# Kernel tuning notes

Measured on AMD Instinct MI355X. Metric: run time of the kernel, lower is better.

## Reference

```python
import jax, jax.numpy as jnp
import numpy as np

B, S, D = 2, 2048, 4096
NH, NKV = 32, 8
HD = D // NH          # 128
NREP = NH // NKV      # 4
SCALE = HD ** -0.5


def setup_inputs() -> dict:
    key = jax.random.key(0)
    kx, kq, kk, kv, ko = jax.random.split(key, 5)
    s = 0.02
    return {
        "x": jax.random.normal(kx, (B, S, D), dtype=jnp.float32),
        "wq": jax.random.normal(kq, (D, NH * HD), dtype=jnp.float32) * s,
        "wk": jax.random.normal(kk, (D, NKV * HD), dtype=jnp.float32) * s,
        "wv": jax.random.normal(kv, (D, NKV * HD), dtype=jnp.float32) * s,
        "wo": jax.random.normal(ko, (NH * HD, D), dtype=jnp.float32) * s,
    }


def reference(x, wq, wk, wv, wo):
    b, s, _ = x.shape
    q = (x @ wq).reshape(b, s, NH, HD)    # b s h d
    k = (x @ wk).reshape(b, s, NKV, HD)   # b s kv d
    v = (x @ wv).reshape(b, s, NKV, HD)
    # GQA: repeat kv heads to match query heads
    k = jnp.repeat(k, NREP, axis=2)       # b s h d
    v = jnp.repeat(v, NREP, axis=2)
    scores = jnp.einsum("bihd,bjhd->bhij", q, k) * SCALE  # b h i j
    causal = jnp.tril(jnp.ones((s, s), dtype=bool))
    scores = jnp.where(causal, scores, jnp.finfo(scores.dtype).min)
    attn = jax.nn.softmax(scores, axis=-1)
    out = jnp.einsum("bhij,bjhd->bihd", attn, v)          # b s h d
    out = out.reshape(b, s, NH * HD)
    return out @ wo
```

## Files before the change

kernel.cpp:

```cpp
#include <hip/hip_runtime.h>
#include <cstdint>
#include <cstddef>

typedef __bf16 bf16x8 __attribute__((ext_vector_type(8)));
typedef float  f32x4  __attribute__((ext_vector_type(4)));
typedef unsigned short u16;

#define SCALE_F 0.08838834764831845f
#define QSCALE_F (0.08838834764831845f * 1.4426950408889634f)

__device__ __forceinline__ u16 f2bf(float f) {
  unsigned int u = __builtin_bit_cast(unsigned int, f);
  u += 0x7fffu + ((u >> 16) & 1u);
  return (u16)(u >> 16);
}

__device__ __forceinline__ unsigned cvt_pk_bf16(float lo, float hi) {
  unsigned r;
  asm("v_cvt_pk_bf16_f32 %0, %1, %2" : "=v"(r) : "v"(lo), "v"(hi));
  return r;
}

__device__ __forceinline__ void load_lds16(const void* g, void* l) {
  __builtin_amdgcn_global_load_lds((const __attribute__((address_space(1))) void*)g,
                                   (__attribute__((address_space(3))) void*)l,
                                   16, 0, 0);
}

__global__ __launch_bounds__(256) void prep_all(const float* __restrict__ x,
                                                const float* __restrict__ wq,
                                                const float* __restrict__ wk,
                                                const float* __restrict__ wv,
                                                const float* __restrict__ wo,
                                                u16* __restrict__ xb,
                                                u16* __restrict__ wqT,
                                                u16* __restrict__ wkvT,
                                                u16* __restrict__ woT) {
  __shared__ float tile[64][33];
  const int tid = threadIdx.x;
  int blk = blockIdx.x;
  if (blk < 2048) {
    int idx = blk * 256 + tid;
    const int n4 = 4096 * 4096 / 4;
    for (; idx < n4; idx += 2048 * 256) {
      float4 v = ((const float4*)x)[idx];
      uint2 pk;
      pk.x = (unsigned)f2bf(v.x) | ((unsigned)f2bf(v.y) << 16);
      pk.y = (unsigned)f2bf(v.z) | ((unsigned)f2bf(v.w) << 16);
      ((uint2*)xb)[idx] = pk;
    }
    return;
  }
  blk -= 2048;
  const float* in; u16* out; long C; int nbx; float scale;
  if (blk < 8192)       { in = wq; out = wqT;                           C = 4096; nbx = 128; scale = QSCALE_F; }
  else if (blk < 10240) { blk -= 8192;  in = wk; out = wkvT;                          C = 1024; nbx = 32; scale = 1.f; }
  else if (blk < 12288) { blk -= 10240; in = wv; out = wkvT + (size_t)1024 * 4096;    C = 1024; nbx = 32; scale = 1.f; }
  else                  { blk -= 12288; in = wo; out = woT;                           C = 4096; nbx = 128; scale = 1.f; }
  const long R = 4096;
  const long c0 = (long)(blk % nbx) * 32, r0 = (long)(blk / nbx) * 64;
  {
    const int tx = tid & 31, ty = tid >> 5;
#pragma unroll
    for (int i = 0; i < 8; i++)
      tile[ty + i * 8][tx] = in[(r0 + ty + i * 8) * C + c0 + tx];
  }
  __syncthreads();
  {
    const int tx = tid & 31, cy = tid >> 5;
#pragma unroll
    for (int i = 0; i < 4; i++) {
      int col = cy + i * 8;
      unsigned val = (unsigned)f2bf(tile[2 * tx][col] * scale) |
                     ((unsigned)f2bf(tile[2 * tx + 1][col] * scale) << 16);
      *(unsigned*)&out[(c0 + col) * R + r0 + 2 * tx] = val;
    }
  }
}

__global__ __launch_bounds__(256) void transpose_u16(const u16* __restrict__ in,
                                                     u16* __restrict__ out,
                                                     int R, int C, int ldi, int ldo) {
  __shared__ u16 tile[32][33];
  const int tx = threadIdx.x, ty = threadIdx.y;
  const long c0 = (long)blockIdx.x * 32, r0 = (long)blockIdx.y * 32;
#pragma unroll
  for (int i = 0; i < 4; i++)
    tile[ty + i * 8][tx] = in[(r0 + ty + i * 8) * (long)ldi + c0 + tx];
  __syncthreads();
#pragma unroll
  for (int i = 0; i < 4; i++)
    out[(c0 + ty + i * 8) * (long)ldo + r0 + tx] = tile[tx][ty + i * 8];
}

template <int BF16_OUT>
__global__ __launch_bounds__(256) void gemm_bt(const u16* __restrict__ A,
                                               const u16* __restrict__ Bt,
                                               void* __restrict__ Cv,
                                               int M, int N, int K) {
  __shared__ u16 As[128 * 32];
  __shared__ u16 Bs[128 * 32];
  const int tid = threadIdx.x;
  const int lane = tid & 63;
  const int g = lane >> 4, r16 = lane & 15;
  const int wid = tid >> 6;
  const int wr = wid >> 1, wc = wid & 1;
  const long bm = (long)blockIdx.y * 128, bn = (long)blockIdx.x * 128;

  const u16* gA = A + (bm + (tid >> 2)) * (long)K + (tid & 3) * 8;
  const u16* gB = Bt + (bn + (tid >> 2)) * (long)K + (tid & 3) * 8;
  u16* lA = As + tid * 8;
  u16* lB = Bs + tid * 8;

  f32x4 acc[4][4];
#pragma unroll
  for (int m = 0; m < 4; m++)
#pragma unroll
    for (int n = 0; n < 4; n++)
#pragma unroll
      for (int j = 0; j < 4; j++) acc[m][n][j] = 0.f;

  for (int k0 = 0; k0 < K; k0 += 32) {
    load_lds16(gA + k0, lA);
    load_lds16(gA + 64 * (long)K + k0, lA + 256 * 8);
    load_lds16(gB + k0, lB);
    load_lds16(gB + 64 * (long)K + k0, lB + 256 * 8);
    __syncthreads();
    bf16x8 af[4], bfr[4];
#pragma unroll
    for (int m = 0; m < 4; m++)
      af[m] = *(const bf16x8*)(As + (wr * 64 + m * 16 + r16) * 32 + g * 8);
#pragma unroll
    for (int n = 0; n < 4; n++)
      bfr[n] = *(const bf16x8*)(Bs + (wc * 64 + n * 16 + r16) * 32 + g * 8);
#pragma unroll
    for (int m = 0; m < 4; m++)
#pragma unroll
      for (int n = 0; n < 4; n++)
        acc[m][n] = __builtin_amdgcn_mfma_f32_16x16x32_bf16(af[m], bfr[n], acc[m][n], 0, 0, 0);
    __syncthreads();
  }

  const long crow = bm + wr * 64 + g * 4;
  const long ccol = bn + wc * 64 + r16;
  if (BF16_OUT) {
    u16* C = (u16*)Cv;
#pragma unroll
    for (int m = 0; m < 4; m++)
#pragma unroll
      for (int n = 0; n < 4; n++)
#pragma unroll
        for (int j = 0; j < 4; j++)
          C[(crow + m * 16 + j) * (long)N + ccol + n * 16] = f2bf(acc[m][n][j]);
  } else {
    float* C = (float*)Cv;
#pragma unroll
    for (int m = 0; m < 4; m++)
#pragma unroll
      for (int n = 0; n < 4; n++)
#pragma unroll
        for (int j = 0; j < 4; j++)
          C[(crow + m * 16 + j) * (long)N + ccol + n * 16] = acc[m][n][j];
  }
}

#define STGA(db, ks, KC) { int kc_ = (KC) < K ? (KC) : 0; \
    load_lds16(gA0 + kc_, &SA[db][ks][s0 * 8]); \
    load_lds16(gA1 + kc_, &SA[db][ks][s1 * 8]); }
#define STGB(db, ks, KC) { int kc_ = (KC) < K ? (KC) : 0; \
    load_lds16(gB0 + kc_, &SB[db][ks][s0 * 8]); \
    load_lds16(gB1 + kc_, &SB[db][ks][s1 * 8]); }

#define PH(MBc, AU, BU, DBn, KSn, MBn, AN, RDB, BN_, STG, DOVM) { \
    STG; \
    if (DOVM) asm volatile("s_waitcnt vmcnt(8)"); \
    __builtin_amdgcn_s_barrier(); \
    _Pragma("unroll") for (int mm = 0; mm < 4; mm++) \
      AN[mm] = *(const bf16x8*)(&SA[DBn][KSn][aoff + (MBn + mm) * 512]); \
    if (RDB) { \
      _Pragma("unroll") for (int n = 0; n < 4; n++) \
        BN_[n] = *(const bf16x8*)(&SB[DBn][KSn][boff + n * 512]); \
    } \
    __builtin_amdgcn_s_setprio(1); \
    _Pragma("unroll") for (int mm = 0; mm < 4; mm++) \
      _Pragma("unroll") for (int n = 0; n < 4; n++) \
        acc[MBc + mm][n] = __builtin_amdgcn_mfma_f32_16x16x32_bf16(AU[mm], BU[n], acc[MBc + mm][n], 0, 0, 0); \
    __builtin_amdgcn_s_setprio(0); \
  }

template <int BF16_OUT>
__device__ __forceinline__ void gemm_body(const u16* __restrict__ A,
                                          const u16* __restrict__ Bt,
                                          void* __restrict__ Cv,
                                          int M, int N, int K, int NBX) {
  __shared__ u16 SA[2][2][8192];
  __shared__ u16 SB[2][2][8192];
  const int tid = threadIdx.x;
  const int lane = tid & 63;
  const int g = lane >> 4, r16 = lane & 15;
  const int wid = tid >> 6;
  const int wm = wid >> 2, wn = wid & 3;

  const int cpx = gridDim.x >> 3;
  const int lin = (blockIdx.x & 7) * cpx + (blockIdx.x >> 3);
  const long bm = (long)(lin / NBX) * 256;
  const long bn = (long)(lin % NBX) * 256;

  const int s0 = tid, s1 = 512 + tid;
  const int rp0 = s0 >> 3, ci0 = (s0 & 7) ^ (rp0 & 7);
  const int rp1 = s1 >> 3, ci1 = (s1 & 7) ^ (rp1 & 7);
  const long gr0 = rp0 * 2 + (ci0 >> 2), gc0 = (ci0 & 3) * 8;
  const long gr1 = rp1 * 2 + (ci1 >> 2), gc1 = (ci1 & 3) * 8;
  const u16* gA0 = A + (bm + gr0) * K + gc0;
  const u16* gA1 = A + (bm + gr1) * K + gc1;
  const u16* gB0 = Bt + (bn + gr0) * K + gc0;
  const u16* gB1 = Bt + (bn + gr1) * K + gc1;

  const int rA = wm * 128 + r16;
  const int aoff = (rA >> 1) * 64 + ((((rA & 1) << 2) + g) ^ ((rA >> 1) & 7)) * 8;
  const int rB = wn * 64 + r16;
  const int boff = (rB >> 1) * 64 + ((((rB & 1) << 2) + g) ^ ((rB >> 1) & 7)) * 8;

  f32x4 acc[8][4];
#pragma unroll
  for (int m = 0; m < 8; m++)
#pragma unroll
    for (int n = 0; n < 4; n++)
#pragma unroll
      for (int j = 0; j < 4; j++) acc[m][n][j] = 0.f;

  bf16x8 afrX[4], afrY[4], bfrX[4], bfrY[4];

  STGA(0, 0, 0); STGB(0, 0, 0);
  STGA(0, 1, 32); STGB(0, 1, 32);
  STGA(1, 0, 64); STGB(1, 0, 64);
  __builtin_amdgcn_sched_barrier(0);
  asm volatile("s_waitcnt vmcnt(0)" ::: "memory");
  __builtin_amdgcn_s_barrier();

#pragma unroll
  for (int mm = 0; mm < 4; mm++)
    afrX[mm] = *(const bf16x8*)(&SA[0][0][aoff + mm * 512]);
#pragma unroll
  for (int n = 0; n < 4; n++)
    bfrX[n] = *(const bf16x8*)(&SB[0][0][boff + n * 512]);

  for (int it = 0; it < K / 128; it++) {
    const int t0 = it * 128;
    PH(0, afrX, bfrX, 0, 0, 4, afrY, 0, bfrY, STGA(1, 1, t0 + 96), 0);
    PH(4, afrY, bfrX, 0, 1, 0, afrX, 1, bfrY, STGB(1, 1, t0 + 96), 1);
    PH(0, afrX, bfrY, 0, 1, 4, afrY, 0, bfrX, STGA(0, 0, t0 + 128), 0);
    PH(4, afrY, bfrY, 1, 0, 0, afrX, 1, bfrX, STGB(0, 0, t0 + 128), 1);
    PH(0, afrX, bfrX, 1, 0, 4, afrY, 0, bfrY, STGA(0, 1, t0 + 160), 0);
    PH(4, afrY, bfrX, 1, 1, 0, afrX, 1, bfrY, STGB(0, 1, t0 + 160), 1);
    PH(0, afrX, bfrY, 1, 1, 4, afrY, 0, bfrX, STGA(1, 0, t0 + 192), 0);
    PH(4, afrY, bfrY, 0, 0, 0, afrX, 1, bfrX, STGB(1, 0, t0 + 192), 1);
  }

  const long crow = bm + wm * 128 + g * 4;
  const long ccol = bn + wn * 64 + r16;
  if (BF16_OUT) {
    u16* C = (u16*)Cv;
#pragma unroll
    for (int m = 0; m < 8; m++)
#pragma unroll
      for (int n = 0; n < 4; n++)
#pragma unroll
        for (int j = 0; j < 4; j++)
          C[(crow + m * 16 + j) * (long)N + ccol + n * 16] = f2bf(acc[m][n][j]);
  } else {
    float* C = (float*)Cv;
#pragma unroll
    for (int m = 0; m < 8; m++)
#pragma unroll
      for (int n = 0; n < 4; n++)
#pragma unroll
        for (int j = 0; j < 4; j++)
          C[(crow + m * 16 + j) * (long)N + ccol + n * 16] = acc[m][n][j];
  }
}

__global__ __launch_bounds__(512, 2) void gemm_q(const u16* __restrict__ A,
                                                 const u16* __restrict__ Bt,
                                                 void* __restrict__ Cv,
                                                 int M, int N, int K, int NBX) {
  gemm_body<1>(A, Bt, Cv, M, N, K, NBX);
}
__global__ __launch_bounds__(512, 2) void gemm_wo(const u16* __restrict__ A,
                                                  const u16* __restrict__ Bt,
                                                  void* __restrict__ Cv,
                                                  int M, int N, int K, int NBX) {
  gemm_body<0>(A, Bt, Cv, M, N, K, NBX);
}

__global__ __launch_bounds__(512, 2) void attn_fwd(const u16* __restrict__ Q,
                                                   const u16* __restrict__ KV,
                                                   const u16* __restrict__ VT,
                                                   u16* __restrict__ Og) {
  __shared__ u16 Ks[2][64 * 128];
  __shared__ u16 Vs[2][128 * 64];
  __shared__ u16 Ps[8][2][16 * 64];
  const int tid = threadIdx.x;
  const int lane = tid & 63;
  const int w = tid >> 6;
  const int g = lane >> 4, r16 = lane & 15;
  const int qtA = blockIdx.x;
  const int qtB = 15 - qtA;
  const int h2 = blockIdx.y, b = blockIdx.z;
  const int h0 = h2 * 2;
  const int kvh = h0 >> 2;

  const u16* kcol   = KV + (long)b * 2048 * 2048 + kvh * 128;
  const u16* vb_ptr = VT + (long)kvh * 128 * 4096 + (long)b * 2048;

  const int nktA = 2 * (qtA + 1);
  const int ntot = 34;

  int qbase = qtA * 128;
  int qlo = qbase + w * 16;
  int qrow = qlo + r16;

  bf16x8 qf[2][4];
  auto load_q = [&]() {
    const u16* qp = Q + ((long)(b * 2048 + qrow)) * 4096 + h0 * 128 + g * 8;
#pragma unroll
    for (int hh = 0; hh < 2; hh++)
#pragma unroll
      for (int kc = 0; kc < 4; kc++)
        qf[hh][kc] = *(const bf16x8*)(qp + hh * 128 + kc * 32);
  };
  load_q();

  f32x4 oacc[2][8];
  float mrun[2], lrun[2];
  auto reinit = [&]() {
#pragma unroll
    for (int hh = 0; hh < 2; hh++) {
#pragma unroll
      for (int dt = 0; dt < 8; dt++)
#pragma unroll
        for (int j = 0; j < 4; j++) oacc[hh][dt][j] = 0.f;
      mrun[hh] = -__builtin_inff();
      lrun[hh] = 0.f;
    }
  };
  reinit();

  auto finalize = [&]() {
#pragma unroll
    for (int hh = 0; hh < 2; hh++) {
      float li[4];
#pragma unroll
      for (int j = 0; j < 4; j++)
        li[j] = 1.f / __shfl(lrun[hh], (lane & 48) + g * 4 + j);
      u16* op = Og + ((long)(b * 2048 + qbase + w * 16 + g * 4)) * 4096 + (h0 + hh) * 128 + r16;
#pragma unroll
      for (int dt = 0; dt < 8; dt++)
#pragma unroll
        for (int j = 0; j < 4; j++)
          op[(long)j * 4096 + dt * 16] = f2bf(oacc[hh][dt][j] * li[j]);
    }
  };

  auto stage = [&](int bf, int kb) {
#pragma unroll
    for (int i = 0; i < 2; i++) {
      int slot = i * 512 + tid;
      int r = slot >> 4, cs = slot & 15;
      int ck = (cs & 8) | ((cs ^ r) & 7);
      load_lds16(kcol + (long)(kb + r) * 2048 + ck * 8, &Ks[bf][slot * 8]);
      int d = slot >> 3, c8 = slot & 7;
      int cv = (c8 ^ d) & 7;
      load_lds16(vb_ptr + (long)d * 4096 + kb + cv * 8, &Vs[bf][slot * 8]);
    }
  };

  stage(0, 0);
  __syncthreads();
  int cur = 0;

  for (int i = 0; i < ntot; i++) {
    if (i == nktA) {
      finalize();
      qbase = qtB * 128;
      qlo = qbase + w * 16;
      qrow = qlo + r16;
      load_q();
      reinit();
    }
    const int kt = (i < nktA) ? i : i - nktA;
    const int kb = kt * 64;
    if (i + 1 < ntot) {
      const int ktn = (i + 1 < nktA) ? i + 1 : i + 1 - nktA;
      stage(cur ^ 1, ktn * 64);
    }

    if (kb <= qlo + 15) {
      const bool masked = (kb + 63 > qlo);

#pragma unroll
      for (int hh = 0; hh < 2; hh++) {
        f32x4 st[4];
#pragma unroll
        for (int t = 0; t < 4; t++)
#pragma unroll
          for (int j = 0; j < 4; j++) st[t][j] = 0.f;
#pragma unroll
        for (int t = 0; t < 4; t++) {
          const int r = t * 16 + r16;
#pragma unroll
          for (int kc = 0; kc < 4; kc++) {
            int c = kc * 4 + g;
            int cz = (c & 8) | ((c ^ r) & 7);
            bf16x8 kf = *(const bf16x8*)(&Ks[cur][r * 128 + cz * 8]);
            st[t] = __builtin_amdgcn_mfma_f32_16x16x32_bf16(kf, qf[hh][kc], st[t], 0, 0, 0);
          }
        }

        float p[4][4];
        float tmax = -__builtin_inff();
#pragma unroll
        for (int t = 0; t < 4; t++)
#pragma unroll
          for (int j = 0; j < 4; j++) {
            float s = st[t][j];
            if (masked) {
              int kv = kb + t * 16 + g * 4 + j;
              s = (kv > qrow) ? -__builtin_inff() : s;
            }
            p[t][j] = s;
            tmax = fmaxf(tmax, s);
          }
        tmax = fmaxf(tmax, __shfl_xor(tmax, 16));
        tmax = fmaxf(tmax, __shfl_xor(tmax, 32));

        if (!__all(tmax <= mrun[hh] + 8.f)) {
          const float mnew = fmaxf(mrun[hh], tmax);
          const float esc = exp2f(mrun[hh] - mnew);
          float es[4];
#pragma unroll
          for (int j = 0; j < 4; j++) es[j] = __shfl(esc, (lane & 48) + g * 4 + j);
#pragma unroll
          for (int dt = 0; dt < 8; dt++)
#pragma unroll
            for (int j = 0; j < 4; j++) oacc[hh][dt][j] *= es[j];
          lrun[hh] *= esc;
          mrun[hh] = mnew;
        }
        float psum = 0.f;
#pragma unroll
        for (int t = 0; t < 4; t++)
#pragma unroll
          for (int j = 0; j < 4; j++) {
            float e = exp2f(p[t][j] - mrun[hh]);
            p[t][j] = e;
            psum += e;
          }
        psum += __shfl_xor(psum, 16);
        psum += __shfl_xor(psum, 32);
        lrun[hh] += psum;

        u16* pw = Ps[w][hh];
#pragma unroll
        for (int t = 0; t < 4; t++)
#pragma unroll
          for (int pp = 0; pp < 2; pp++) {
            int kvl = t * 16 + g * 4 + pp * 2;
            unsigned val = cvt_pk_bf16(p[t][pp * 2], p[t][pp * 2 + 1]);
            int off = r16 * 128 + ((kvl * 2) ^ ((r16 & 7) << 4));
            *(unsigned int*)((char*)pw + off) = val;
          }

#pragma unroll
        for (int kc2 = 0; kc2 < 2; kc2++) {
          int c = kc2 * 4 + g;
          int cp = c ^ (r16 & 7);
          bf16x8 pa = *(const bf16x8*)(pw + r16 * 64 + cp * 8);
#pragma unroll
          for (int dt = 0; dt < 8; dt++) {
            int d = dt * 16 + r16;
            int cz = c ^ (d & 7);
            bf16x8 vf = *(const bf16x8*)(&Vs[cur][d * 64 + cz * 8]);
            oacc[hh][dt] = __builtin_amdgcn_mfma_f32_16x16x32_bf16(pa, vf, oacc[hh][dt], 0, 0, 0);
          }
        }
      }
    }

    __syncthreads();
    cur ^= 1;
  }

  finalize();
}

extern "C" void kernel_launch(void* const* d_in, const int* in_sizes, int n_in,
                              void* d_out, int out_size, void* d_ws, size_t ws_size,
                              hipStream_t stream) {
  (void)in_sizes; (void)n_in; (void)out_size; (void)ws_size;
  const float* x  = (const float*)d_in[0];
  const float* wq = (const float*)d_in[1];
  const float* wk = (const float*)d_in[2];
  const float* wv = (const float*)d_in[3];
  const float* wo = (const float*)d_in[4];
  float* out = (float*)d_out;

  u16* xb    = (u16*)d_ws;
  u16* wqT   = xb   + (size_t)4096 * 4096;
  u16* wkvT  = wqT  + (size_t)4096 * 4096;
  u16* woT   = wkvT + (size_t)2048 * 4096;
  u16* qb    = woT  + (size_t)4096 * 4096;
  u16* kvb   = qb   + (size_t)4096 * 4096;
  u16* vT    = kvb  + (size_t)4096 * 2048;
  u16* attn  = xb;

  prep_all<<<22528, 256, 0, stream>>>(x, wq, wk, wv, wo, xb, wqT, wkvT, woT);

  gemm_q<<<256, 512, 0, stream>>>(xb, wqT, qb, 4096, 4096, 4096, 16);
  gemm_bt<1><<<dim3(16, 32), 256, 0, stream>>>(xb, wkvT, kvb, 4096, 2048, 4096);
  transpose_u16<<<dim3(32, 128), dim3(32, 8), 0, stream>>>(kvb + 1024, vT, 4096, 1024, 2048, 4096);

  attn_fwd<<<dim3(8, 16, 2), 512, 0, stream>>>(qb, kvb, vT, attn);

  gemm_wo<<<256, 512, 0, stream>>>(attn, woT, out, 4096, 4096, 4096, 16);
}
```

Before: 529.6 us.

## Process one head per attention block instead of two, doubling grid

Each attention block used to handle two query heads that share a KV head. It now handles a single head, with half the Q registers, output accumulators and P scratch in LDS, and the grid doubles to 512 blocks. Launch bounds are raised to 4 blocks per SM to improve occupancy and latency hiding. The cost is that K/V tiles are loaded twice as often, since sibling heads no longer share a staged tile.

```diff
diff --git a/kernel.cpp b/kernel.cpp
--- a/kernel.cpp
+++ b/kernel.cpp
@@ -293,25 +293,25 @@
   gemm_body<0>(A, Bt, Cv, M, N, K, NBX);
 }
 
-__global__ __launch_bounds__(512, 2) void attn_fwd(const u16* __restrict__ Q,
+__global__ __launch_bounds__(512, 4) void attn_fwd(const u16* __restrict__ Q,
                                                    const u16* __restrict__ KV,
                                                    const u16* __restrict__ VT,
                                                    u16* __restrict__ Og) {
   __shared__ u16 Ks[2][64 * 128];
   __shared__ u16 Vs[2][128 * 64];
-  __shared__ u16 Ps[8][2][16 * 64];
+  __shared__ u16 Ps[8][16 * 64];
   const int tid = threadIdx.x;
   const int lane = tid & 63;
   const int w = tid >> 6;
   const int g = lane >> 4, r16 = lane & 15;
   const int qtA = blockIdx.x;
   const int qtB = 15 - qtA;
-  const int h2 = blockIdx.y, b = blockIdx.z;
-  const int h0 = h2 * 2;
-  const int kvh = h0 >> 2;
+  const int h = blockIdx.y, b = blockIdx.z;
+  const int kvh = h >> 2;
 
   const u16* kcol   = KV + (long)b * 2048 * 2048 + kvh * 128;
   const u16* vb_ptr = VT + (long)kvh * 128 * 4096 + (long)b * 2048;
+  u16* pw = Ps[w];
 
   const int nktA = 2 * (qtA + 1);
   const int ntot = 34;
@@ -320,46 +320,37 @@
   int qlo = qbase + w * 16;
   int qrow = qlo + r16;
 
-  bf16x8 qf[2][4];
+  bf16x8 qf[4];
   auto load_q = [&]() {
-    const u16* qp = Q + ((long)(b * 2048 + qrow)) * 4096 + h0 * 128 + g * 8;
-#pragma unroll
-    for (int hh = 0; hh < 2; hh++)
-#pragma unroll
-      for (int kc = 0; kc < 4; kc++)
-        qf[hh][kc] = *(const bf16x8*)(qp + hh * 128 + kc * 32);
+    const u16* qp = Q + ((long)(b * 2048 + qrow)) * 4096 + h * 128 + g * 8;
+#pragma unroll
+    for (int kc = 0; kc < 4; kc++) qf[kc] = *(const bf16x8*)(qp + kc * 32);
   };
   load_q();
 
-  f32x4 oacc[2][8];
-  float mrun[2], lrun[2];
+  f32x4 oacc[8];
+  float mrun, lrun;
   auto reinit = [&]() {
 #pragma unroll
-    for (int hh = 0; hh < 2; hh++) {
-#pragma unroll
-      for (int dt = 0; dt < 8; dt++)
-#pragma unroll
-        for (int j = 0; j < 4; j++) oacc[hh][dt][j] = 0.f;
-      mrun[hh] = -__builtin_inff();
-      lrun[hh] = 0.f;
-    }
+    for (int dt = 0; dt < 8; dt++)
+#pragma unroll
+      for (int j = 0; j < 4; j++) oacc[dt][j] = 0.f;
+    mrun = -__builtin_inff();
+    lrun = 0.f;
   };
   reinit();
 
   auto finalize = [&]() {
-#pragma unroll
-    for (int hh = 0; hh < 2; hh++) {
-      float li[4];
+    float li[4];
+#pragma unroll
+    for (int j = 0; j < 4; j++)
+      li[j] = 1.f / __shfl(lrun, (lane & 48) + g * 4 + j);
+    u16* op = Og + ((long)(b * 2048 + qbase + w * 16 + g * 4)) * 4096 + h * 128 + r16;
+#pragma unroll
+    for (int dt = 0; dt < 8; dt++)
 #pragma unroll
       for (int j = 0; j < 4; j++)
-        li[j] = 1.f / __shfl(lrun[hh], (lane & 48) + g * 4 + j);
-      u16* op = Og + ((long)(b * 2048 + qbase + w * 16 + g * 4)) * 4096 + (h0 + hh) * 128 + r16;
-#pragma unroll
-      for (int dt = 0; dt < 8; dt++)
-#pragma unroll
-        for (int j = 0; j < 4; j++)
-          op[(long)j * 4096 + dt * 16] = f2bf(oacc[hh][dt][j] * li[j]);
-    }
+        op[(long)j * 4096 + dt * 16] = f2bf(oacc[dt][j] * li[j]);
   };
 
   auto stage = [&](int bf, int kb) {
@@ -398,91 +389,87 @@
     if (kb <= qlo + 15) {
       const bool masked = (kb + 63 > qlo);
 
-#pragma unroll
-      for (int hh = 0; hh < 2; hh++) {
-        f32x4 st[4];
-#pragma unroll
-        for (int t = 0; t < 4; t++)
-#pragma unroll
-          for (int j = 0; j < 4; j++) st[t][j] = 0.f;
-#pragma unroll
-        for (int t = 0; t < 4; t++) {
-          const int r = t * 16 + r16;
-#pragma unroll
-          for (int kc = 0; kc < 4; kc++) {
-            int c = kc * 4 + g;
-            int cz = (c & 8) | ((c ^ r) & 7);
-            bf16x8 kf = *(const bf16x8*)(&Ks[cur][r * 128 + cz * 8]);
-            st[t] = __builtin_amdgcn_mfma_f32_16x16x32_bf16(kf, qf[hh][kc], st[t], 0, 0, 0);
+      f32x4 st[4];
+#pragma unroll
+      for (int t = 0; t < 4; t++)
+#pragma unroll
+        for (int j = 0; j < 4; j++) st[t][j] = 0.f;
+#pragma unroll
+      for (int t = 0; t < 4; t++) {
+        const int r = t * 16 + r16;
+#pragma unroll
+        for (int kc = 0; kc < 4; kc++) {
+          int c = kc * 4 + g;
+          int cz = (c & 8) | ((c ^ r) & 7);
+          bf16x8 kf = *(const bf16x8*)(&Ks[cur][r * 128 + cz * 8]);
+          st[t] = __builtin_amdgcn_mfma_f32_16x16x32_bf16(kf, qf[kc], st[t], 0, 0, 0);
+        }
+      }
+
+      float p[4][4];
+      float tmax = -__builtin_inff();
+#pragma unroll
+      for (int t = 0; t < 4; t++)
+#pragma unroll
+        for (int j = 0; j < 4; j++) {
+          float s = st[t][j];
+          if (masked) {
+            int kv = kb + t * 16 + g * 4 + j;
+            s = (kv > qrow) ? -__builtin_inff() : s;
           }
+          p[t][j] = s;
+          tmax = fmaxf(tmax, s);
         }
-
-        float p[4][4];
-        float tmax = -__builtin_inff();
-#pragma unroll
-        for (int t = 0; t < 4; t++)
-#pragma unroll
-          for (int j = 0; j < 4; j++) {
-            float s = st[t][j];
-            if (masked) {
-              int kv = kb + t * 16 + g * 4 + j;
-              s = (kv > qrow) ? -__builtin_inff() : s;
-            }
-            p[t][j] = s;
-            tmax = fmaxf(tmax, s);
-          }
-        tmax = fmaxf(tmax, __shfl_xor(tmax, 16));
-        tmax = fmaxf(tmax, __shfl_xor(tmax, 32));
-
-        if (!__all(tmax <= mrun[hh] + 8.f)) {
-          const float mnew = fmaxf(mrun[hh], tmax);
-          const float esc = exp2f(mrun[hh] - mnew);
-          float es[4];
-#pragma unroll
-          for (int j = 0; j < 4; j++) es[j] = __shfl(esc, (lane & 48) + g * 4 + j);
-#pragma unroll
-          for (int dt = 0; dt < 8; dt++)
-#pragma unroll
-            for (int j = 0; j < 4; j++) oacc[hh][dt][j] *= es[j];
-          lrun[hh] *= esc;
-          mrun[hh] = mnew;
+      tmax = fmaxf(tmax, __shfl_xor(tmax, 16));
+      tmax = fmaxf(tmax, __shfl_xor(tmax, 32));
+
+      if (!__all(tmax <= mrun + 8.f)) {
+        const float mnew = fmaxf(mrun, tmax);
+        const float esc = exp2f(mrun - mnew);
+        float es[4];
+#pragma unroll
+        for (int j = 0; j < 4; j++) es[j] = __shfl(esc, (lane & 48) + g * 4 + j);
+#pragma unroll
+        for (int dt = 0; dt < 8; dt++)
+#pragma unroll
+          for (int j = 0; j < 4; j++) oacc[dt][j] *= es[j];
+        lrun *= esc;
+        mrun = mnew;
+      }
+      float psum = 0.f;
+#pragma unroll
+      for (int t = 0; t < 4; t++)
+#pragma unroll
+        for (int j = 0; j < 4; j++) {
+          float e = exp2f(p[t][j] - mrun);
+          p[t][j] = e;
+          psum += e;
         }
-        float psum = 0.f;
-#pragma unroll
-        for (int t = 0; t < 4; t++)
-#pragma unroll
-          for (int j = 0; j < 4; j++) {
-            float e = exp2f(p[t][j] - mrun[hh]);
-            p[t][j] = e;
-            psum += e;
-          }
-        psum += __shfl_xor(psum, 16);
-        psum += __shfl_xor(psum, 32);
-        lrun[hh] += psum;
-
-        u16* pw = Ps[w][hh];
-#pragma unroll
-        for (int t = 0; t < 4; t++)
-#pragma unroll
-          for (int pp = 0; pp < 2; pp++) {
-            int kvl = t * 16 + g * 4 + pp * 2;
-            unsigned val = cvt_pk_bf16(p[t][pp * 2], p[t][pp * 2 + 1]);
-            int off = r16 * 128 + ((kvl * 2) ^ ((r16 & 7) << 4));
-            *(unsigned int*)((char*)pw + off) = val;
-          }
-
-#pragma unroll
-        for (int kc2 = 0; kc2 < 2; kc2++) {
-          int c = kc2 * 4 + g;
-          int cp = c ^ (r16 & 7);
-          bf16x8 pa = *(const bf16x8*)(pw + r16 * 64 + cp * 8);
-#pragma unroll
-          for (int dt = 0; dt < 8; dt++) {
-            int d = dt * 16 + r16;
-            int cz = c ^ (d & 7);
-            bf16x8 vf = *(const bf16x8*)(&Vs[cur][d * 64 + cz * 8]);
-            oacc[hh][dt] = __builtin_amdgcn_mfma_f32_16x16x32_bf16(pa, vf, oacc[hh][dt], 0, 0, 0);
-          }
+      psum += __shfl_xor(psum, 16);
+      psum += __shfl_xor(psum, 32);
+      lrun += psum;
+
+#pragma unroll
+      for (int t = 0; t < 4; t++)
+#pragma unroll
+        for (int pp = 0; pp < 2; pp++) {
+          int kvl = t * 16 + g * 4 + pp * 2;
+          unsigned val = cvt_pk_bf16(p[t][pp * 2], p[t][pp * 2 + 1]);
+          int off = r16 * 128 + ((kvl * 2) ^ ((r16 & 7) << 4));
+          *(unsigned int*)((char*)pw + off) = val;
+        }
+
+#pragma unroll
+      for (int kc2 = 0; kc2 < 2; kc2++) {
+        int c = kc2 * 4 + g;
+        int cp = c ^ (r16 & 7);
+        bf16x8 pa = *(const bf16x8*)(pw + r16 * 64 + cp * 8);
+#pragma unroll
+        for (int dt = 0; dt < 8; dt++) {
+          int d = dt * 16 + r16;
+          int cz = c ^ (d & 7);
+          bf16x8 vf = *(const bf16x8*)(&Vs[cur][d * 64 + cz * 8]);
+          oacc[dt] = __builtin_amdgcn_mfma_f32_16x16x32_bf16(pa, vf, oacc[dt], 0, 0, 0);
         }
       }
     }
@@ -520,7 +507,7 @@
   gemm_bt<1><<<dim3(16, 32), 256, 0, stream>>>(xb, wkvT, kvb, 4096, 2048, 4096);
   transpose_u16<<<dim3(32, 128), dim3(32, 8), 0, stream>>>(kvb + 1024, vT, 4096, 1024, 2048, 4096);
 
-  attn_fwd<<<dim3(8, 16, 2), 512, 0, stream>>>(qb, kvb, vT, attn);
+  attn_fwd<<<dim3(8, 32, 2), 512, 0, stream>>>(qb, kvb, vT, attn);
 
   gemm_wo<<<256, 512, 0, stream>>>(attn, woT, out, 4096, 4096, 4096, 16);
 }
```

Result: no change. 534.4 us (+0.9%).
